# Kernel tuning notes

Measured on AMD Instinct MI355X. Metric: run time of the kernel, lower is better.

## Reference

```python
import jax, jax.numpy as jnp
import numpy as np

B = 256; NROIS = 200; IN = 200; HID = 128; L = 4; H = 8; RATIO = 0.5
K = int(np.ceil(RATIO * NROIS))        # SAGPooling top-k per graph = 100
N = B * NROIS                          # total nodes = 51200
DEG = 32; EPG = NROIS * DEG; E_EDGES = B * EPG  # 1,638,400 edges
EMB = HID * L                          # MHA embed dim = 512
DH = EMB // H

def _xavier(k, shape):
    fan_in, fan_out = shape[-2], shape[-1]
    lim = float(np.sqrt(6.0 / (fan_in + fan_out)))
    return jax.random.uniform(k, shape, jnp.float32, -lim, lim)

def setup_inputs() -> dict:
    key = jax.random.key(0)
    ks = jax.random.split(key, 16)
    x = jax.random.normal(ks[0], (N, IN), jnp.float32)
    # block-diagonal edge list: edges stay within each graph's node range
    src = jax.random.randint(ks[1], (E_EDGES,), 0, NROIS, jnp.int32)
    dst = jax.random.randint(ks[2], (E_EDGES,), 0, NROIS, jnp.int32)
    off = jnp.repeat(jnp.arange(B, dtype=jnp.int32) * NROIS, EPG)
    edge_index = jnp.stack([src + off, dst + off])
    edge_attr = jax.random.normal(ks[3], (E_EDGES,), jnp.float32)  # unused by the math
    batch = jnp.repeat(jnp.arange(B, dtype=jnp.int32), NROIS)
    return dict(
        x=x, edge_index=edge_index, edge_attr=edge_attr, batch=batch,
        gcn_w0=_xavier(ks[4], (IN, HID)),
        gcn_w=_xavier(ks[5], (L - 1, HID, HID)),
        gcn_b=jnp.zeros((L, HID), jnp.float32),
        lin1_w0=_xavier(ks[6], (IN + HID, HID)),
        lin1_w=_xavier(ks[7], (L - 1, 2 * HID, HID)),
        lin1_b=jnp.zeros((L, HID), jnp.float32),
        lin2_w=_xavier(ks[8], (L, HID, HID)),
        lin2_b=jnp.zeros((L, HID), jnp.float32),
        sag_w1=_xavier(ks[9], (HID, 1)),
        sag_w2=_xavier(ks[10], (HID, 1)),
        sag_b=jnp.zeros((1,), jnp.float32),
        mha_in_w=_xavier(ks[11], (3 * EMB, EMB)),
        mha_in_b=jnp.zeros((3 * EMB,), jnp.float32),
        mha_out_w=_xavier(ks[12], (EMB, EMB)),
        mha_out_b=jnp.zeros((EMB,), jnp.float32),
        fin_w=_xavier(ks[13], (EMB, HID)),
        fin_b=jnp.zeros((HID,), jnp.float32),
    )

def _gcn_conv(x, src, dst, W, b):
    xw = x @ W
    deg = jax.ops.segment_sum(jnp.ones_like(dst, jnp.float32), dst, num_segments=N) + 1.0
    dinv = jax.lax.rsqrt(deg)
    norm = dinv[src] * dinv[dst]                     # [E]
    agg = jax.ops.segment_sum(xw[src] * norm[:, None], dst, num_segments=N)
    agg = agg + xw * (dinv * dinv)[:, None]          # self-loop term
    return agg + b

def _gcblock(x, src, dst, gw, gb, l1w, l1b, l2w, l2b):
    x1 = jnp.tanh(_gcn_conv(x, src, dst, gw, gb))
    h = jnp.tanh(jnp.concatenate([x, x1], axis=1) @ l1w + l1b)
    return jnp.tanh(h @ l2w + l2b)

def _sag_pool_pad(z, src, dst, w1, w2, b):
    # SAGPooling score via PyG GraphConv (aggr='add'): lin_rel(sum_j x_j) + lin_root(x_i)
    neigh = jax.ops.segment_sum(z[src], dst, num_segments=N)
    score = (neigh @ w1)[:, 0] + b[0] + (z @ w2)[:, 0]        # [N]
    s3 = score.reshape(B, NROIS)
    vals, idx = jax.lax.top_k(s3, K)                           # [B,K]
    z3 = z.reshape(B, NROIS, HID)
    pooled = jnp.take_along_axis(z3, idx[:, :, None], axis=1) * jnp.tanh(vals)[:, :, None]
    zpad = jnp.zeros_like(z3).at[jnp.arange(B)[:, None], idx].set(pooled)
    return zpad.reshape(N, HID)

def reference(x, edge_index, edge_attr, batch,
              gcn_w0, gcn_w, gcn_b, lin1_w0, lin1_w, lin1_b, lin2_w, lin2_b,
              sag_w1, sag_w2, sag_b,
              mha_in_w, mha_in_b, mha_out_w, mha_out_b, fin_w, fin_b):
    src, dst = edge_index[0], edge_index[1]
    z = x
    pads = []
    for i in range(L):
        gw = gcn_w0 if i == 0 else gcn_w[i - 1]
        l1w = lin1_w0 if i == 0 else lin1_w[i - 1]
        z = _gcblock(z, src, dst, gw, gcn_b[i], l1w, lin1_b[i], lin2_w[i], lin2_b[i])
        pads.append(_sag_pool_pad(z, src, dst, sag_w1, sag_w2, sag_b))
    xc = jnp.concatenate(pads, axis=1).reshape(B, NROIS, EMB)   # [B,S,E]
    # MultiheadAttention (batch_first, eval mode -> no dropout)
    qkv = xc @ mha_in_w.T + mha_in_b                             # [B,S,3E]
    q, k, v = jnp.split(qkv, 3, axis=-1)
    def heads(t):
        return t.reshape(B, NROIS, H, DH).transpose(0, 2, 1, 3)  # [B,H,S,dh]
    q, k, v = heads(q), heads(k), heads(v)
    scores = jnp.einsum('bhqd,bhkd->bhqk', q, k) / np.sqrt(DH)
    attn = jax.nn.softmax(scores, axis=-1)                       # [B,H,S,S]
    o = jnp.einsum('bhqk,bhkd->bhqd', attn, v).transpose(0, 2, 1, 3).reshape(B, NROIS, EMB)
    o = o @ mha_out_w.T + mha_out_b
    attn_weights = attn.mean(axis=1)                             # avg over heads [B,S,S]
    # readout: global_mean_pool over each graph's nrois nodes
    pooled = o.mean(axis=1)                                      # [B,E]
    out = jnp.tanh(pooled @ fin_w + fin_b)                       # [B,HID]
    return out, attn_weights
```

## Files before the change

### kernel.cpp

```cpp
#include <hip/hip_runtime.h>
#include <hip/hip_fp16.h>


#define GB   256
#define SS   200
#define KIN  200
#define HD   128
#define NLAY 4
#define NHD  8
#define TOPK 100
#define NT   (GB * SS)
#define EPG_ 6400
#define NE_  (GB * EPG_)
#define EMB_ 512

typedef _Float16 half8 __attribute__((ext_vector_type(8)));
typedef _Float16 half4v __attribute__((ext_vector_type(4)));
typedef float floatx4 __attribute__((ext_vector_type(4)));

__global__ __launch_bounds__(256) void k_build_A(const int* __restrict__ src,
                                                 const int* __restrict__ dst,
                                                 float* __restrict__ A) {
  int e = blockIdx.x * 256 + threadIdx.x;
  if (e >= NE_) return;
  int d = dst[e], s = src[e];
  int b = d / SS;
  int dl = d - b * SS;
  int sl = s - b * SS;
  atomicAdd(&A[((size_t)b * SS + dl) * SS + sl], 1.0f);
}

__global__ __launch_bounds__(256) void k_dinv(const float* __restrict__ A,
                                              float* __restrict__ dinv) {
  int node = blockIdx.x * 4 + (threadIdx.x >> 6);
  int lane = threadIdx.x & 63;
  const float* r = A + (size_t)node * SS;
  float v = r[lane] + r[lane + 64] + r[lane + 128];
  if (lane < 8) v += r[lane + 192];
#pragma unroll
  for (int o = 32; o; o >>= 1) v += __shfl_xor(v, o);
  if (lane == 0) dinv[node] = rsqrtf(v + 1.0f);
}

__global__ __launch_bounds__(256) void k_prep_all(
    const float* __restrict__ gcn_w0, const float* __restrict__ gcn_w,
    const float* __restrict__ lin1_w0, const float* __restrict__ lin1_w,
    const float* __restrict__ lin2_w,
    __half* __restrict__ whi, __half* __restrict__ wlo) {
  const int mat = blockIdx.x >> 7;
  const int n   = blockIdx.x & 127;
  const int l = mat / 3, which = mat % 3;
  const float* src;
  int K, Kpad;
  if (which == 0) {
    K = l ? HD : KIN;  Kpad = l ? 128 : 256;
    src = l ? gcn_w + (size_t)(l - 1) * HD * HD : gcn_w0;
  } else if (which == 1) {
    K = l ? 2 * HD : KIN + HD;  Kpad = l ? 256 : 384;
    src = l ? lin1_w + (size_t)(l - 1) * 2 * HD * HD : lin1_w0;
  } else {
    K = HD;  Kpad = HD;
    src = lin2_w + (size_t)l * HD * HD;
  }
  int off = (l == 0) ? (which == 0 ? 0 : (which == 1 ? 32768 : 81920))
                     : 98304 + (l - 1) * 65536 +
                       (which == 0 ? 0 : (which == 1 ? 16384 : 49152));
  _Float16* wh = (_Float16*)whi + (size_t)off + (size_t)n * Kpad;
  _Float16* wl = (_Float16*)wlo + (size_t)off + (size_t)n * Kpad;
  for (int k = threadIdx.x; k < Kpad; k += 256) {
    float v = (k < K) ? src[(size_t)k * HD + n] : 0.f;
    _Float16 h = (_Float16)v;
    wh[k] = h;
    wl[k] = (_Float16)(v - (float)h);
  }
}

__global__ __launch_bounds__(256) void k_prep_w16(const float* __restrict__ W,
                                                  __half* __restrict__ W16) {
  int i = blockIdx.x * 256 + threadIdx.x;
  float4 v = reinterpret_cast<const float4*>(W)[i];
  half4v h = {(_Float16)v.x, (_Float16)v.y, (_Float16)v.z, (_Float16)v.w};
  *reinterpret_cast<half4v*>((_Float16*)W16 + (size_t)i * 4) = h;
}

__global__ __launch_bounds__(256) void k_node_mfma(
    const float* __restrict__ in1, int k1,
    const float* __restrict__ in2,
    const __half* __restrict__ Whi, const __half* __restrict__ Wlo,
    int Kpad,
    const float* __restrict__ bias,
    float* __restrict__ out, int doTanh) {
  const int m0 = blockIdx.x * 64;
  const int t = threadIdx.x;
  const int wave = t >> 6, lane = t & 63;
  const int col = lane & 15, quad = lane >> 4;
  const int wm = (wave & 1) * 32;
  const int wn = (wave >> 1) * 64;
  __shared__ __align__(16) _Float16 Ah[64][72];
  __shared__ __align__(16) _Float16 Al[64][72];
  floatx4 acc[2][4] = {};
  const int lr = t >> 2;
  const int lk = (t & 3) * 16;
  const _Float16* Wh = (const _Float16*)Whi;
  const _Float16* Wl = (const _Float16*)Wlo;

  for (int k0 = 0; k0 < Kpad; k0 += 64) {
    __syncthreads();
#pragma unroll
    for (int q = 0; q < 4; ++q) {
      int kg = k0 + lk + q * 4;
      float4 v = {0.f, 0.f, 0.f, 0.f};
      if (kg < k1)
        v = *reinterpret_cast<const float4*>(&in1[(size_t)(m0 + lr) * k1 + kg]);
      else if (in2 && kg < k1 + HD)
        v = *reinterpret_cast<const float4*>(&in2[(size_t)(m0 + lr) * HD + (kg - k1)]);
      half4v h = {(_Float16)v.x, (_Float16)v.y, (_Float16)v.z, (_Float16)v.w};
      half4v lo = {(_Float16)(v.x - (float)h.x), (_Float16)(v.y - (float)h.y),
                   (_Float16)(v.z - (float)h.z), (_Float16)(v.w - (float)h.w)};
      *reinterpret_cast<half4v*>(&Ah[lr][lk + q * 4]) = h;
      *reinterpret_cast<half4v*>(&Al[lr][lk + q * 4]) = lo;
    }
    __syncthreads();
#pragma unroll
    for (int ks = 0; ks < 2; ++ks) {
      half8 ah[2], al[2], bh[4], bl[4];
#pragma unroll
      for (int i = 0; i < 2; ++i) {
        ah[i] = *reinterpret_cast<const half8*>(&Ah[wm + i * 16 + col][ks * 32 + quad * 8]);
        al[i] = *reinterpret_cast<const half8*>(&Al[wm + i * 16 + col][ks * 32 + quad * 8]);
      }
#pragma unroll
      for (int j = 0; j < 4; ++j) {
        const size_t wo = (size_t)(wn + j * 16 + col) * Kpad + k0 + ks * 32 + quad * 8;
        bh[j] = *reinterpret_cast<const half8*>(Wh + wo);
        bl[j] = *reinterpret_cast<const half8*>(Wl + wo);
      }
#pragma unroll
      for (int i = 0; i < 2; ++i)
#pragma unroll
        for (int j = 0; j < 4; ++j) {
          acc[i][j] = __builtin_amdgcn_mfma_f32_16x16x32_f16(ah[i], bh[j], acc[i][j], 0, 0, 0);
          acc[i][j] = __builtin_amdgcn_mfma_f32_16x16x32_f16(ah[i], bl[j], acc[i][j], 0, 0, 0);
          acc[i][j] = __builtin_amdgcn_mfma_f32_16x16x32_f16(al[i], bh[j], acc[i][j], 0, 0, 0);
        }
    }
  }
#pragma unroll
  for (int j = 0; j < 4; ++j) {
    int n = wn + j * 16 + col;
    float bb = bias ? bias[n] : 0.f;
#pragma unroll
    for (int i = 0; i < 2; ++i) {
      int rbase = m0 + wm + i * 16 + quad * 4;
#pragma unroll
      for (int r = 0; r < 4; ++r) {
        float v = acc[i][j][r] + bb;
        if (doTanh) v = tanhf(v);
        out[(size_t)(rbase + r) * HD + n] = v;
      }
    }
  }
}

__global__ __launch_bounds__(256) void k_agg_mfma(
    const float* __restrict__ A, const float* __restrict__ dinv,
    const float* __restrict__ xw, const float* __restrict__ bias,
    float* __restrict__ out) {
  const int b    = blockIdx.x >> 1;
  const int row0 = (blockIdx.x & 1) * 128;
  const int t = threadIdx.x;
  const int wave = t >> 6, lane = t & 63;
  const int col = lane & 15, quad = lane >> 4;
  const int wm = (wave & 1) * 64, wn = (wave >> 1) * 64;
  __shared__ __align__(16) _Float16 Ah[128][72];
  __shared__ __align__(16) _Float16 Al[128][72];
  __shared__ __align__(16) _Float16 Bh[128][72];
  __shared__ __align__(16) _Float16 Bl[128][72];
  __shared__ float dvs[256];
  dvs[t] = (t < SS) ? dinv[b * SS + t] : 0.f;
  floatx4 acc[4][4] = {};
  const float* Ab  = A  + (size_t)b * SS * SS;
  const float* xwb = xw + (size_t)b * SS * HD;
  const int lr = t >> 1, lk = (t & 1) * 32;
  const int d = row0 + lr;
  __syncthreads();
  const float dvd = (d < SS) ? dvs[d] : 0.f;

  for (int k0 = 0; k0 < 256; k0 += 64) {
    __syncthreads();
#pragma unroll
    for (int q = 0; q < 8; ++q) {
      int s = k0 + lk + q * 4;
      float4 v = {0.f, 0.f, 0.f, 0.f};
      if (d < SS && s < SS)
        v = *reinterpret_cast<const float4*>(&Ab[(size_t)d * SS + s]);
      float e0 = (v.x + ((s + 0 == d) ? 1.f : 0.f)) * dvd * dvs[(s + 0) & 255];
      float e1 = (v.y + ((s + 1 == d) ? 1.f : 0.f)) * dvd * dvs[(s + 1) & 255];
      float e2 = (v.z + ((s + 2 == d) ? 1.f : 0.f)) * dvd * dvs[(s + 2) & 255];
      float e3 = (v.w + ((s + 3 == d) ? 1.f : 0.f)) * dvd * dvs[(s + 3) & 255];
      half4v h = {(_Float16)e0, (_Float16)e1, (_Float16)e2, (_Float16)e3};
      half4v lo = {(_Float16)(e0 - (float)h.x), (_Float16)(e1 - (float)h.y),
                   (_Float16)(e2 - (float)h.z), (_Float16)(e3 - (float)h.w)};
      *reinterpret_cast<half4v*>(&Ah[lr][lk + q * 4]) = h;
      *reinterpret_cast<half4v*>(&Al[lr][lk + q * 4]) = lo;
    }
#pragma unroll
    for (int p = 0; p < 8; ++p) {
      int idx = t + p * 256;
      int c4 = idx & 31, ss = idx >> 5;
      int s = k0 + ss;
      float4 v = {0.f, 0.f, 0.f, 0.f};
      if (s < SS)
        v = *reinterpret_cast<const float4*>(&xwb[(size_t)s * HD + c4 * 4]);
      int ssx = ss ^ ((c4 & 7) << 3);
      float e[4] = {v.x, v.y, v.z, v.w};
#pragma unroll
      for (int j = 0; j < 4; ++j) {
        _Float16 h = (_Float16)e[j];
        Bh[c4 * 4 + j][ssx] = h;
        Bl[c4 * 4 + j][ssx] = (_Float16)(e[j] - (float)h);
      }
    }
    __syncthreads();
#pragma unroll
    for (int ks = 0; ks < 2; ++ks) {
      half8 ah[4], al[4], bh[4], bl[4];
#pragma unroll
      for (int i = 0; i < 4; ++i) {
        ah[i] = *reinterpret_cast<const half8*>(&Ah[wm + i * 16 + col][ks * 32 + quad * 8]);
        al[i] = *reinterpret_cast<const half8*>(&Al[wm + i * 16 + col][ks * 32 + quad * 8]);
      }
#pragma unroll
      for (int j = 0; j < 4; ++j) {
        int n = wn + j * 16 + col;
        int koff = (ks * 32 + quad * 8) ^ (((n >> 2) & 7) << 3);
        bh[j] = *reinterpret_cast<const half8*>(&Bh[n][koff]);
        bl[j] = *reinterpret_cast<const half8*>(&Bl[n][koff]);
      }
#pragma unroll
      for (int i = 0; i < 4; ++i)
#pragma unroll
        for (int j = 0; j < 4; ++j) {
          acc[i][j] = __builtin_amdgcn_mfma_f32_16x16x32_f16(ah[i], bh[j], acc[i][j], 0, 0, 0);
          acc[i][j] = __builtin_amdgcn_mfma_f32_16x16x32_f16(ah[i], bl[j], acc[i][j], 0, 0, 0);
          acc[i][j] = __builtin_amdgcn_mfma_f32_16x16x32_f16(al[i], bh[j], acc[i][j], 0, 0, 0);
        }
    }
  }
#pragma unroll
  for (int j = 0; j < 4; ++j) {
    int n = wn + j * 16 + col;
    float bb = bias[n];
#pragma unroll
    for (int i = 0; i < 4; ++i) {
      int rbase = row0 + wm + i * 16 + quad * 4;
#pragma unroll
      for (int r = 0; r < 4; ++r) {
        int row = rbase + r;
        if (row < SS)
          out[((size_t)b * SS + row) * HD + n] = tanhf(acc[i][j][r] + bb);
      }
    }
  }
}

__global__ __launch_bounds__(256) void k_sag(
    const float* __restrict__ z, const float* __restrict__ A,
    const float* __restrict__ w1, const float* __restrict__ w2,
    const float* __restrict__ sb,
    __half* __restrict__ xch, __half* __restrict__ xcl, int layer) {
  const int b = blockIdx.x, t = threadIdx.x;
  __shared__ float w1s[HD], w2s[HD];
  __shared__ float zw1[SS], sc[SS], fac[SS];
  if (t < HD) { w1s[t] = w1[t]; w2s[t] = w2[t]; }
  __syncthreads();
  float a2 = 0.f;
  if (t < SS) {
    const float4* zr = reinterpret_cast<const float4*>(&z[((size_t)b * SS + t) * HD]);
    float a1 = 0.f;
#pragma unroll
    for (int q = 0; q < HD / 4; ++q) {
      float4 v = zr[q];
      a1 += v.x * w1s[4 * q] + v.y * w1s[4 * q + 1] + v.z * w1s[4 * q + 2] + v.w * w1s[4 * q + 3];
      a2 += v.x * w2s[4 * q] + v.y * w2s[4 * q + 1] + v.z * w2s[4 * q + 2] + v.w * w2s[4 * q + 3];
    }
    zw1[t] = a1;
  }
  __syncthreads();
  if (t < SS) {
    float s = sb[0] + a2;
    const float4* ar = reinterpret_cast<const float4*>(&A[((size_t)b * SS + t) * SS]);
#pragma unroll 5
    for (int q = 0; q < SS / 4; ++q) {
      float4 v = ar[q];
      s += v.x * zw1[4 * q] + v.y * zw1[4 * q + 1] + v.z * zw1[4 * q + 2] + v.w * zw1[4 * q + 3];
    }
    sc[t] = s;
  }
  __syncthreads();
  if (t < SS) {
    float si = sc[t];
    int cnt = 0;
    for (int j = 0; j < SS; ++j) {
      float sj = sc[j];
      cnt += (sj > si || (sj == si && j < t)) ? 1 : 0;
    }
    fac[t] = (cnt < TOPK) ? tanhf(si) : 0.f;
  }
  __syncthreads();
  _Float16* xh = (_Float16*)xch;
  _Float16* xl = (_Float16*)xcl;
  for (int idx = t; idx < SS * HD; idx += 256) {
    int row = idx >> 7, c = idx & 127;
    float v = fac[row] * z[((size_t)b * SS + row) * HD + c];
    _Float16 h = (_Float16)v;
    size_t o = ((size_t)b * SS + row) * EMB_ + layer * HD + c;
    xh[o] = h;
    xl[o] = (_Float16)(v - (float)h);
  }
}

__global__ __launch_bounds__(256) void k_proj(
    const __half* __restrict__ xch, const __half* __restrict__ Win16,
    const float* __restrict__ bin, __half* __restrict__ QKh) {
  const int wg = (blockIdx.x & 7) * 400 + (blockIdx.x >> 3);
  const int bm = wg >> 3;
  const int bn = wg & 7;
  const int m0 = bm * 128, n0 = bn * 128;
  const int t = threadIdx.x;
  const int wave = t >> 6, lane = t & 63;
  const int col = lane & 15, quad = lane >> 4;
  const int wm = (wave & 1) * 64;
  const int wn = (wave >> 1) * 64;
  __shared__ __align__(16) _Float16 As[128][64];
  __shared__ __align__(16) _Float16 Bs[128][64];
  floatx4 acc[4][4] = {};
  const _Float16* X = (const _Float16*)xch;
  const _Float16* W = (const _Float16*)Win16;

  const int srow = lane >> 3;
  const int sch  = (lane & 7) ^ srow;
  const int arow = wave * 8 + srow;
  const int fsw = col & 7;

  for (int k0 = 0; k0 < EMB_; k0 += 64) {
#pragma unroll
    for (int q = 0; q < 4; ++q) {
      const _Float16* ga = X + (size_t)(m0 + q * 32 + arow) * EMB_ + k0 + sch * 8;
      __builtin_amdgcn_global_load_lds(
          (const __attribute__((address_space(1))) void*)ga,
          (__attribute__((address_space(3))) void*)((char*)&As[0][0] + q * 4096 + wave * 1024),
          16, 0, 0);
      const _Float16* gb = W + (size_t)(n0 + q * 32 + arow) * EMB_ + k0 + sch * 8;
      __builtin_amdgcn_global_load_lds(
          (const __attribute__((address_space(1))) void*)gb,
          (__attribute__((address_space(3))) void*)((char*)&Bs[0][0] + q * 4096 + wave * 1024),
          16, 0, 0);
    }
    __syncthreads();
#pragma unroll
    for (int ks = 0; ks < 2; ++ks) {
      const int ch = (ks * 4 + quad) ^ fsw;
      half8 af[4], bf[4];
#pragma unroll
      for (int i = 0; i < 4; ++i)
        af[i] = *reinterpret_cast<const half8*>(
            (const char*)&As[0][0] + (wm + i * 16 + col) * 128 + ch * 16);
#pragma unroll
      for (int j = 0; j < 4; ++j)
        bf[j] = *reinterpret_cast<const half8*>(
            (const char*)&Bs[0][0] + (wn + j * 16 + col) * 128 + ch * 16);
#pragma unroll
      for (int i = 0; i < 4; ++i)
#pragma unroll
        for (int j = 0; j < 4; ++j)
          acc[i][j] = __builtin_amdgcn_mfma_f32_16x16x32_f16(af[i], bf[j], acc[i][j], 0, 0, 0);
    }
    __syncthreads();
  }
#pragma unroll
  for (int j = 0; j < 4; ++j) {
    int c = n0 + wn + j * 16 + col;
    float bb = bin[c];
#pragma unroll
    for (int i = 0; i < 4; ++i) {
      int rbase = m0 + wm + i * 16 + quad * 4;
#pragma unroll
      for (int r = 0; r < 4; ++r)
        QKh[(size_t)(rbase + r) * 1024 + c] = __float2half(acc[i][j][r] + bb);
    }
  }
}

__global__ __launch_bounds__(256) void k_attn(
    const __half* __restrict__ QKh,
    float* __restrict__ cpbuf,
    float* __restrict__ attn) {
  const int bx = (blockIdx.x & 7) * 416 + (blockIdx.x >> 3);
  const int b  = bx / 13;
  const int it = bx % 13;
  const int i0 = it * 16;
  const int rows = (SS - i0 >= 16) ? 16 : (SS - i0);
  const int t    = threadIdx.x;
  const int wave = t >> 6;
  const int lane = t & 63;
  const int col  = lane & 15;
  const int quad = lane >> 4;

  __shared__ __align__(16) float Ss[16][212];

  float am[13];
  int   soff[13];
  int   kmax = 0;
#pragma unroll
  for (int k = 0; k < 13; ++k) {
    int idx = t + (k << 8);
    am[k] = 0.f;
    if (idx < rows * 200) {
      int i = idx / 200;
      soff[k] = idx + 12 * i;
      kmax = k + 1;
    } else soff[k] = 0;
  }

  const _Float16* Qbase = (const _Float16*)QKh + (size_t)b * SS * 1024;
  const _Float16* qrow = Qbase + (size_t)(i0 + col) * 1024 + quad * 8;
  const _Float16* krow[4];
#pragma unroll
  for (int m = 0; m < 4; ++m) {
    int jt = wave + m * 4;
    krow[m] = Qbase + (size_t)(jt * 16 + col) * 1024 + 512 + quad * 8;
  }

  for (int h = 0; h < NHD; ++h) {
    const int hoff = h * 64;
    half8 a0 = *reinterpret_cast<const half8*>(qrow + hoff);
    half8 a1 = *reinterpret_cast<const half8*>(qrow + hoff + 32);
#pragma unroll
    for (int m = 0; m < 4; ++m) {
      int jt = wave + m * 4;
      if (jt < 13) {
        half8 b0 = *reinterpret_cast<const half8*>(krow[m] + hoff);
        half8 b1 = *reinterpret_cast<const half8*>(krow[m] + hoff + 32);
        floatx4 acc = {0.f, 0.f, 0.f, 0.f};
        acc = __builtin_amdgcn_mfma_f32_16x16x32_f16(a0, b0, acc, 0, 0, 0);
        acc = __builtin_amdgcn_mfma_f32_16x16x32_f16(a1, b1, acc, 0, 0, 0);
#pragma unroll
        for (int r = 0; r < 4; ++r)
          Ss[quad * 4 + r][jt * 16 + col] = acc[r] * 0.125f;
      }
    }
    __syncthreads();
#pragma unroll
    for (int ri = 0; ri < 4; ++ri) {
      int r = wave * 4 + ri;
      if (r < rows) {
        float* srow = &Ss[r][0];
        float s0 = srow[lane], s1 = srow[lane + 64], s2 = srow[lane + 128];
        float s3 = (lane < 8) ? srow[lane + 192] : -1e30f;
        float mx = fmaxf(fmaxf(s0, s1), fmaxf(s2, s3));
#pragma unroll
        for (int o = 32; o; o >>= 1) mx = fmaxf(mx, __shfl_xor(mx, o));
        float e0 = __expf(s0 - mx), e1 = __expf(s1 - mx), e2 = __expf(s2 - mx);
        float e3 = (lane < 8) ? __expf(s3 - mx) : 0.f;
        float sum = e0 + e1 + e2 + e3;
#pragma unroll
        for (int o = 32; o; o >>= 1) sum += __shfl_xor(sum, o);
        float rl = 1.0f / sum;
        srow[lane] = e0 * rl; srow[lane + 64] = e1 * rl; srow[lane + 128] = e2 * rl;
        if (lane < 8) srow[lane + 192] = e3 * rl;
      }
    }
    __syncthreads();
    const float* sflat = &Ss[0][0];
#pragma unroll
    for (int k = 0; k < 13; ++k)
      if (k < kmax) am[k] += sflat[soff[k]] * 0.125f;
    if (t < SS) {
      float s = 0.f;
      for (int i = 0; i < rows; ++i) s += Ss[i][t];
      atomicAdd(&cpbuf[((size_t)b * NHD + h) * SS + t], s);
    }
    __syncthreads();
  }
  float* abase = &attn[((size_t)b * SS + i0) * SS];
#pragma unroll
  for (int k = 0; k < 13; ++k)
    if (k < kmax) abase[t + (k << 8)] = am[k];
}

__global__ __launch_bounds__(256) void k_pool(
    const __half* __restrict__ xch, const __half* __restrict__ xcl,
    const float* __restrict__ cpbuf,
    const float* __restrict__ Win, const float* __restrict__ bin,
    float* __restrict__ pooled) {
  const int b = blockIdx.x, t = threadIdx.x;
  __shared__ float cps[NHD][SS];
  __shared__ float tvs[NHD][EMB_];
  for (int idx = t; idx < NHD * SS; idx += 256) {
    int h = idx / SS, j = idx - h * SS;
    cps[h][j] = cpbuf[((size_t)b * NHD + h) * SS + j];
  }
  __syncthreads();
  const _Float16* xh = (const _Float16*)xch + (size_t)b * SS * EMB_;
  const _Float16* xl = (const _Float16*)xcl + (size_t)b * SS * EMB_;
  float a0[NHD] = {0.f}, a1[NHD] = {0.f};
  for (int j = 0; j < SS; ++j) {
    float x0 = (float)xh[(size_t)j * EMB_ + t] + (float)xl[(size_t)j * EMB_ + t];
    float x1 = (float)xh[(size_t)j * EMB_ + t + 256] + (float)xl[(size_t)j * EMB_ + t + 256];
#pragma unroll
    for (int h = 0; h < NHD; ++h) {
      float c = cps[h][j];
      a0[h] += c * x0; a1[h] += c * x1;
    }
  }
#pragma unroll
  for (int h = 0; h < NHD; ++h) { tvs[h][t] = a0[h]; tvs[h][t + 256] = a1[h]; }
  __syncthreads();
  const int wv = t >> 6, lane = t & 63;
  for (int e = wv; e < EMB_; e += 4) {
    int h = e >> 6;
    const float* wr = Win + (size_t)(2 * EMB_ + e) * EMB_;
    float s = 0.f;
#pragma unroll
    for (int q = 0; q < 8; ++q) s += wr[lane + q * 64] * tvs[h][lane + q * 64];
#pragma unroll
    for (int o = 32; o; o >>= 1) s += __shfl_xor(s, o);
    if (lane == 0) pooled[(size_t)b * EMB_ + e] = bin[2 * EMB_ + e] * (float)SS + s;
  }
}

__global__ __launch_bounds__(256) void k_final(
    const float* __restrict__ pooled, const float* __restrict__ Wout,
    const float* __restrict__ bout, const float* __restrict__ finw,
    const float* __restrict__ finb, float* __restrict__ out) {
  const int b = blockIdx.x, t = threadIdx.x;
  __shared__ float pl[EMB_], po[EMB_];
  for (int k = t; k < EMB_; k += 256) pl[k] = pooled[(size_t)b * EMB_ + k] * (1.0f / (float)SS);
  __syncthreads();
  for (int e = t; e < EMB_; e += 256) {
    const float* wr = &Wout[(size_t)e * EMB_];
    float a = bout[e];
    for (int k = 0; k < EMB_; ++k) a += wr[k] * pl[k];
    po[e] = a;
  }
  __syncthreads();
  if (t < HD) {
    float a = finb[t];
    for (int e = 0; e < EMB_; ++e) a += po[e] * finw[(size_t)e * HD + t];
    out[(size_t)b * HD + t] = tanhf(a);
  }
}

extern "C" void kernel_launch(void* const* d_in, const int* in_sizes, int n_in,
                              void* d_out, int out_size, void* d_ws, size_t ws_size,
                              hipStream_t stream) {
  const float* x         = (const float*)d_in[0];
  const int*   ei        = (const int*)d_in[1];
  const float* gcn_w0    = (const float*)d_in[4];
  const float* gcn_w     = (const float*)d_in[5];
  const float* gcn_b     = (const float*)d_in[6];
  const float* lin1_w0   = (const float*)d_in[7];
  const float* lin1_w    = (const float*)d_in[8];
  const float* lin1_b    = (const float*)d_in[9];
  const float* lin2_w    = (const float*)d_in[10];
  const float* lin2_b    = (const float*)d_in[11];
  const float* sag_w1    = (const float*)d_in[12];
  const float* sag_w2    = (const float*)d_in[13];
  const float* sag_b     = (const float*)d_in[14];
  const float* mha_in_w  = (const float*)d_in[15];
  const float* mha_in_b  = (const float*)d_in[16];
  const float* mha_out_w = (const float*)d_in[17];
  const float* mha_out_b = (const float*)d_in[18];
  const float* fin_w     = (const float*)d_in[19];
  const float* fin_b     = (const float*)d_in[20];

  float* ws     = (float*)d_ws;
  float* dinv   = ws;
  float* Araw   = dinv + NT;
  float* buf0   = Araw + (size_t)GB * SS * SS;
  float* buf1   = buf0 + (size_t)NT * HD;
  float* zbuf   = buf1 + (size_t)NT * HD;
  float* xcf    = zbuf + (size_t)NT * HD;
  __half* xch   = (__half*)xcf;
  __half* xcl   = xch + (size_t)NT * EMB_;
  float* pooled = xcf + (size_t)NT * EMB_;
  __half* QKh  = (__half*)Araw;
  float* cpbuf = Araw + 26214400;

  float* outp = (float*)d_out;
  float* attn = outp + (size_t)GB * HD;

  __half* whi   = (__half*)attn;
  __half* wlo   = whi + 294912;
  __half* Win16 = wlo + 294912;

  hipMemsetAsync(Araw, 0, (size_t)GB * SS * SS * sizeof(float), stream);

  k_prep_all<<<12 * 128, 256, 0, stream>>>(gcn_w0, gcn_w, lin1_w0, lin1_w, lin2_w, whi, wlo);
  k_prep_w16<<<512, 256, 0, stream>>>(mha_in_w, Win16);
  k_build_A<<<NE_ / 256, 256, 0, stream>>>(ei, ei + NE_, Araw);
  k_dinv<<<NT / 4, 256, 0, stream>>>(Araw, dinv);

  static const int KPg[4]  = {256, 128, 128, 128};
  static const int KP1[4]  = {384, 256, 256, 256};
  static const int OFFg[4] = {0, 98304, 163840, 229376};
  static const int OFF1[4] = {32768, 114688, 180224, 245760};
  static const int OFF2[4] = {81920, 147456, 212992, 278528};

  for (int l = 0; l < NLAY; ++l) {
    const float* zin = (l == 0) ? x : zbuf;
    int k1 = (l == 0) ? KIN : HD;
    k_node_mfma<<<NT / 64, 256, 0, stream>>>(zin, k1, nullptr,
                                             whi + OFFg[l], wlo + OFFg[l], KPg[l],
                                             nullptr, buf0, 0);
    k_agg_mfma<<<GB * 2, 256, 0, stream>>>(Araw, dinv, buf0, gcn_b + l * HD, buf1);
    k_node_mfma<<<NT / 64, 256, 0, stream>>>(zin, k1, buf1,
                                             whi + OFF1[l], wlo + OFF1[l], KP1[l],
                                             lin1_b + l * HD, buf0, 1);
    k_node_mfma<<<NT / 64, 256, 0, stream>>>(buf0, HD, nullptr,
                                             whi + OFF2[l], wlo + OFF2[l], HD,
                                             lin2_b + l * HD, zbuf, 1);
    k_sag<<<GB, 256, 0, stream>>>(zbuf, Araw, sag_w1, sag_w2, sag_b, xch, xcl, l);
  }

  hipMemsetAsync(cpbuf, 0, (size_t)GB * NHD * SS * sizeof(float), stream);
  k_proj<<<(NT / 128) * 8, 256, 0, stream>>>(xch, Win16, mha_in_b, QKh);
  k_attn<<<GB * 13, 256, 0, stream>>>(QKh, cpbuf, attn);
  k_pool<<<GB, 256, 0, stream>>>(xch, xcl, cpbuf, mha_in_w, mha_in_b, pooled);
  k_final<<<GB, 256, 0, stream>>>(pooled, mha_out_w, mha_out_b, fin_w, fin_b, outp);
}
```

Before: 1.450 ms.

## Fuse lin1, lin2 and next-layer GCN projection into one kernel per layer

Adds k_fused, which computes lin1 (concat input with aggregated features, tanh), lin2 (tanh) and the next layer's GCN weight projection inside one block. The intermediates stay in LDS as split hi/lo fp16. This replaces three node-GEMM launches per layer with one, cutting global round trips for the intermediate activations and re-reads of z. In exchange it uses more LDS per block, which may lower occupancy, and it reorders the pipeline so the first GCN projection is hoisted out of the loop.

Measured after the change: 1.372 ms. 5.4% less time.

```diff
diff --git a/kernel.cpp b/kernel.cpp
--- a/kernel.cpp
+++ b/kernel.cpp
@@ -157,6 +157,176 @@
         float v = acc[i][j][r] + bb;
         if (doTanh) v = tanhf(v);
         out[(size_t)(rbase + r) * HD + n] = v;
+      }
+    }
+  }
+}
+
+__global__ __launch_bounds__(256) void k_fused(
+    const float* __restrict__ in1, int k1,
+    const float* __restrict__ x1,
+    const __half* __restrict__ l1wh, const __half* __restrict__ l1wl, int KP1,
+    const float* __restrict__ l1b,
+    const __half* __restrict__ l2wh, const __half* __restrict__ l2wl,
+    const float* __restrict__ l2b,
+    const __half* __restrict__ gwh, const __half* __restrict__ gwl,
+    float* __restrict__ zout, float* __restrict__ xwout) {
+  const int m0 = blockIdx.x * 64;
+  const int t = threadIdx.x;
+  const int wave = t >> 6, lane = t & 63;
+  const int col = lane & 15, quad = lane >> 4;
+  const int wm = (wave & 1) * 32;
+  const int wn = (wave >> 1) * 64;
+  __shared__ __align__(16) _Float16 Ah[64][72];
+  __shared__ __align__(16) _Float16 Al[64][72];
+  __shared__ __align__(16) _Float16 Hh[64][136];
+  __shared__ __align__(16) _Float16 Hl[64][136];
+  const int lr = t >> 2;
+  const int lk = (t & 3) * 16;
+
+  {
+    floatx4 acc[2][4] = {};
+    for (int k0 = 0; k0 < KP1; k0 += 64) {
+      __syncthreads();
+#pragma unroll
+      for (int q = 0; q < 4; ++q) {
+        int kg = k0 + lk + q * 4;
+        float4 v = {0.f, 0.f, 0.f, 0.f};
+        if (kg < k1)
+          v = *reinterpret_cast<const float4*>(&in1[(size_t)(m0 + lr) * k1 + kg]);
+        else if (kg < k1 + HD)
+          v = *reinterpret_cast<const float4*>(&x1[(size_t)(m0 + lr) * HD + (kg - k1)]);
+        half4v h = {(_Float16)v.x, (_Float16)v.y, (_Float16)v.z, (_Float16)v.w};
+        half4v lo = {(_Float16)(v.x - (float)h.x), (_Float16)(v.y - (float)h.y),
+                     (_Float16)(v.z - (float)h.z), (_Float16)(v.w - (float)h.w)};
+        *reinterpret_cast<half4v*>(&Ah[lr][lk + q * 4]) = h;
+        *reinterpret_cast<half4v*>(&Al[lr][lk + q * 4]) = lo;
+      }
+      __syncthreads();
+#pragma unroll
+      for (int ks = 0; ks < 2; ++ks) {
+        half8 ah[2], al[2], bh[4], bl[4];
+#pragma unroll
+        for (int i = 0; i < 2; ++i) {
+          ah[i] = *reinterpret_cast<const half8*>(&Ah[wm + i * 16 + col][ks * 32 + quad * 8]);
+          al[i] = *reinterpret_cast<const half8*>(&Al[wm + i * 16 + col][ks * 32 + quad * 8]);
+        }
+#pragma unroll
+        for (int j = 0; j < 4; ++j) {
+          const size_t wo = (size_t)(wn + j * 16 + col) * KP1 + k0 + ks * 32 + quad * 8;
+          bh[j] = *reinterpret_cast<const half8*>((const _Float16*)l1wh + wo);
+          bl[j] = *reinterpret_cast<const half8*>((const _Float16*)l1wl + wo);
+        }
+#pragma unroll
+        for (int i = 0; i < 2; ++i)
+#pragma unroll
+          for (int j = 0; j < 4; ++j) {
+            acc[i][j] = __builtin_amdgcn_mfma_f32_16x16x32_f16(ah[i], bh[j], acc[i][j], 0, 0, 0);
+            acc[i][j] = __builtin_amdgcn_mfma_f32_16x16x32_f16(ah[i], bl[j], acc[i][j], 0, 0, 0);
+            acc[i][j] = __builtin_amdgcn_mfma_f32_16x16x32_f16(al[i], bh[j], acc[i][j], 0, 0, 0);
+          }
+      }
+    }
+#pragma unroll
+    for (int j = 0; j < 4; ++j) {
+      int n = wn + j * 16 + col;
+      float bb = l1b[n];
+#pragma unroll
+      for (int i = 0; i < 2; ++i) {
+        int rb = wm + i * 16 + quad * 4;
+#pragma unroll
+        for (int r = 0; r < 4; ++r) {
+          float v = tanhf(acc[i][j][r] + bb);
+          _Float16 h = (_Float16)v;
+          Hh[rb + r][n] = h;
+          Hl[rb + r][n] = (_Float16)(v - (float)h);
+        }
+      }
+    }
+  }
+  __syncthreads();
+
+  {
+    floatx4 acc[2][4] = {};
+#pragma unroll
+    for (int kc = 0; kc < 4; ++kc) {
+      half8 ah[2], al[2], bh[4], bl[4];
+#pragma unroll
+      for (int i = 0; i < 2; ++i) {
+        ah[i] = *reinterpret_cast<const half8*>(&Hh[wm + i * 16 + col][kc * 32 + quad * 8]);
+        al[i] = *reinterpret_cast<const half8*>(&Hl[wm + i * 16 + col][kc * 32 + quad * 8]);
+      }
+#pragma unroll
+      for (int j = 0; j < 4; ++j) {
+        const size_t wo = (size_t)(wn + j * 16 + col) * HD + kc * 32 + quad * 8;
+        bh[j] = *reinterpret_cast<const half8*>((const _Float16*)l2wh + wo);
+        bl[j] = *reinterpret_cast<const half8*>((const _Float16*)l2wl + wo);
+      }
+#pragma unroll
+      for (int i = 0; i < 2; ++i)
+#pragma unroll
+        for (int j = 0; j < 4; ++j) {
+          acc[i][j] = __builtin_amdgcn_mfma_f32_16x16x32_f16(ah[i], bh[j], acc[i][j], 0, 0, 0);
+          acc[i][j] = __builtin_amdgcn_mfma_f32_16x16x32_f16(ah[i], bl[j], acc[i][j], 0, 0, 0);
+          acc[i][j] = __builtin_amdgcn_mfma_f32_16x16x32_f16(al[i], bh[j], acc[i][j], 0, 0, 0);
+        }
+    }
+    __syncthreads();
+#pragma unroll
+    for (int j = 0; j < 4; ++j) {
+      int n = wn + j * 16 + col;
+      float bb = l2b[n];
+#pragma unroll
+      for (int i = 0; i < 2; ++i) {
+        int rb = wm + i * 16 + quad * 4;
+#pragma unroll
+        for (int r = 0; r < 4; ++r) {
+          float v = tanhf(acc[i][j][r] + bb);
+          zout[(size_t)(m0 + rb + r) * HD + n] = v;
+          _Float16 h = (_Float16)v;
+          Hh[rb + r][n] = h;
+          Hl[rb + r][n] = (_Float16)(v - (float)h);
+        }
+      }
+    }
+  }
+  if (!gwh) return;
+  __syncthreads();
+
+  {
+    floatx4 acc[2][4] = {};
+#pragma unroll
+    for (int kc = 0; kc < 4; ++kc) {
+      half8 ah[2], al[2], bh[4], bl[4];
+#pragma unroll
+      for (int i = 0; i < 2; ++i) {
+        ah[i] = *reinterpret_cast<const half8*>(&Hh[wm + i * 16 + col][kc * 32 + quad * 8]);
+        al[i] = *reinterpret_cast<const half8*>(&Hl[wm + i * 16 + col][kc * 32 + quad * 8]);
+      }
+#pragma unroll
+      for (int j = 0; j < 4; ++j) {
+        const size_t wo = (size_t)(wn + j * 16 + col) * HD + kc * 32 + quad * 8;
+        bh[j] = *reinterpret_cast<const half8*>((const _Float16*)gwh + wo);
+        bl[j] = *reinterpret_cast<const half8*>((const _Float16*)gwl + wo);
+      }
+#pragma unroll
+      for (int i = 0; i < 2; ++i)
+#pragma unroll
+        for (int j = 0; j < 4; ++j) {
+          acc[i][j] = __builtin_amdgcn_mfma_f32_16x16x32_f16(ah[i], bh[j], acc[i][j], 0, 0, 0);
+          acc[i][j] = __builtin_amdgcn_mfma_f32_16x16x32_f16(ah[i], bl[j], acc[i][j], 0, 0, 0);
+          acc[i][j] = __builtin_amdgcn_mfma_f32_16x16x32_f16(al[i], bh[j], acc[i][j], 0, 0, 0);
+        }
+    }
+#pragma unroll
+    for (int j = 0; j < 4; ++j) {
+      int n = wn + j * 16 + col;
+#pragma unroll
+      for (int i = 0; i < 2; ++i) {
+        int rb = wm + i * 16 + quad * 4;
+#pragma unroll
+        for (int r = 0; r < 4; ++r)
+          xwout[(size_t)(m0 + rb + r) * HD + n] = acc[i][j][r];
       }
     }
   }
@@ -602,25 +772,26 @@
   k_build_A<<<NE_ / 256, 256, 0, stream>>>(ei, ei + NE_, Araw);
   k_dinv<<<NT / 4, 256, 0, stream>>>(Araw, dinv);
 
-  static const int KPg[4]  = {256, 128, 128, 128};
   static const int KP1[4]  = {384, 256, 256, 256};
   static const int OFFg[4] = {0, 98304, 163840, 229376};
   static const int OFF1[4] = {32768, 114688, 180224, 245760};
   static const int OFF2[4] = {81920, 147456, 212992, 278528};
 
+  k_node_mfma<<<NT / 64, 256, 0, stream>>>(x, KIN, nullptr,
+                                           whi + OFFg[0], wlo + OFFg[0], 256,
+                                           nullptr, buf0, 0);
+
   for (int l = 0; l < NLAY; ++l) {
     const float* zin = (l == 0) ? x : zbuf;
     int k1 = (l == 0) ? KIN : HD;
-    k_node_mfma<<<NT / 64, 256, 0, stream>>>(zin, k1, nullptr,
-                                             whi + OFFg[l], wlo + OFFg[l], KPg[l],
-                                             nullptr, buf0, 0);
     k_agg_mfma<<<GB * 2, 256, 0, stream>>>(Araw, dinv, buf0, gcn_b + l * HD, buf1);
-    k_node_mfma<<<NT / 64, 256, 0, stream>>>(zin, k1, buf1,
-                                             whi + OFF1[l], wlo + OFF1[l], KP1[l],
-                                             lin1_b + l * HD, buf0, 1);
-    k_node_mfma<<<NT / 64, 256, 0, stream>>>(buf0, HD, nullptr,
-                                             whi + OFF2[l], wlo + OFF2[l], HD,
-                                             lin2_b + l * HD, zbuf, 1);
+    k_fused<<<NT / 64, 256, 0, stream>>>(
+        zin, k1, buf1,
+        whi + OFF1[l], wlo + OFF1[l], KP1[l], lin1_b + l * HD,
+        whi + OFF2[l], wlo + OFF2[l], lin2_b + l * HD,
+        (l < NLAY - 1) ? whi + OFFg[l + 1] : (const __half*)nullptr,
+        (l < NLAY - 1) ? wlo + OFFg[l + 1] : (const __half*)nullptr,
+        zbuf, buf0);
     k_sag<<<GB, 256, 0, stream>>>(zbuf, Araw, sag_w1, sag_w2, sag_b, xch, xcl, l);
   }
 
```
